# Kernel tuning notes

Hardware: AMD Instinct MI355X
Metric: run time of the kernel (lower is better)

## Reference

```python
import jax, jax.numpy as jnp
import numpy as np

DIM = 384
HEADS = 8
HEAD_DIM = DIM // HEADS
TEM_LEN = 400
SCALE = HEAD_DIM ** -0.5


def setup_inputs() -> dict:
    key = jax.random.key(0)
    ks = jax.random.split(key, 12)
    B, Lq, Lkv = 16, 1024, 1424
    inp = {
        'tem_mask': jax.random.normal(ks[0], (B, TEM_LEN, DIM), jnp.float32),
        'search_mask': jax.random.normal(ks[1], (B, Lkv - TEM_LEN, DIM), jnp.float32),
        'q': jax.random.normal(ks[2], (B, Lq, DIM), jnp.float32),
        'kv': jax.random.normal(ks[3], (B, Lkv, DIM), jnp.float32),
        'attn_pos': jax.random.normal(ks[4], (1, HEADS, Lq, Lkv), jnp.float32),
        # learned params (attn_pos_encoding_only=True: q, fused kv, proj)
        'q_w': jax.random.normal(ks[5], (DIM, DIM), jnp.float32) * 0.02,
        'q_b': jnp.zeros((DIM,), jnp.float32),
        'kv_w': jax.random.normal(ks[6], (2 * DIM, DIM), jnp.float32) * 0.02,
        'kv_b': jnp.zeros((2 * DIM,), jnp.float32),
        'proj_w': jax.random.normal(ks[7], (DIM, DIM), jnp.float32) * 0.02,
        'proj_b': jnp.zeros((DIM,), jnp.float32),
    }
    return inp


def reference(tem_mask, search_mask, q, kv, attn_pos, q_w, q_b, kv_w, kv_b, proj_w, proj_b):
    B, Lq, C = q.shape
    Lkv = kv.shape[1]
    # projections
    qh = (q @ q_w.T + q_b).reshape(B, Lq, HEADS, HEAD_DIM).transpose(0, 2, 1, 3)  # (B,H,Lq,hd)
    kvp = kv @ kv_w.T + kv_b                                                      # (B,Lkv,2C)
    k = kvp[..., :C]
    v = kvp[..., C:]
    # additive masks on v before head split (template tokens first, then search)
    v = jnp.concatenate([v[:, :TEM_LEN] + tem_mask, v[:, TEM_LEN:] + search_mask], axis=1)
    kh = k.reshape(B, Lkv, HEADS, HEAD_DIM).transpose(0, 2, 1, 3)  # (B,H,Lkv,hd)
    vh = v.reshape(B, Lkv, HEADS, HEAD_DIM).transpose(0, 2, 1, 3)  # (B,H,Lkv,hd)
    # scaled scores + untied positional bias, softmax over keys
    attn = jnp.einsum('bhqd,bhkd->bhqk', qh, kh) * SCALE + attn_pos
    attn = jax.nn.softmax(attn, axis=-1)
    x = jnp.einsum('bhqk,bhkd->bhqd', attn, vh)
    x = x.transpose(0, 2, 1, 3).reshape(B, Lq, C)
    return x @ proj_w.T + proj_b
```

## Files before the change

kernel.cpp:

```cpp
#include <hip/hip_runtime.h>
#include <stdint.h>

#define NB 16
#define NH 8
#define LQ 1024
#define LKV 1424
#define LKVP 1472
#define DIMC 384
#define NKVT 23
#define TEM 400
#define QSCALE 0.20823509f
#define LOG2E_F 1.4426950408889634f

typedef __attribute__((ext_vector_type(4))) float f32x4;
typedef __attribute__((ext_vector_type(8))) short bf16x8;
typedef __attribute__((ext_vector_type(4))) unsigned short us4;
typedef __attribute__((ext_vector_type(2))) unsigned int u32x2;
typedef __attribute__((ext_vector_type(4))) unsigned int u32x4;

__device__ __forceinline__ unsigned short f2b(float f) {
  unsigned int u = __builtin_bit_cast(unsigned int, f);
  u += 0x7fffu + ((u >> 16) & 1u);
  return (unsigned short)(u >> 16);
}

__device__ __forceinline__ void gload_lds16(const void* gsrc, void* ldst) {
  __builtin_amdgcn_global_load_lds(
      (const __attribute__((address_space(1))) void*)gsrc,
      (__attribute__((address_space(3))) void*)ldst, 16, 0, 0);
}

__global__ __launch_bounds__(256) void conv_all(
    const float* __restrict__ q, const float* __restrict__ kv,
    const float* __restrict__ qw, const float* __restrict__ kvw,
    const float* __restrict__ pw, unsigned short* __restrict__ qb,
    unsigned short* __restrict__ kvb, unsigned short* __restrict__ qwb,
    unsigned short* __restrict__ kvwb, unsigned short* __restrict__ pwb) {
  int i = blockIdx.x * 256 + threadIdx.x;
  const float* src;
  unsigned short* dst;
  if (i < 16384 * 48) { src = q; dst = qb; }
  else if (i < 39168 * 48) { i -= 16384 * 48; src = kv; dst = kvb; }
  else if (i < 39552 * 48) { i -= 39168 * 48; src = qw; dst = qwb; }
  else if (i < 40320 * 48) { i -= 39552 * 48; src = kvw; dst = kvwb; }
  else if (i < 40704 * 48) { i -= 40320 * 48; src = pw; dst = pwb; }
  else return;
  int row = i / 48, ch = i - row * 48;
  const float* sp = src + (size_t)row * DIMC + ch * 8;
  f32x4 x = *(const f32x4*)sp;
  f32x4 y = *(const f32x4*)(sp + 4);
  bf16x8 o;
  o[0] = (short)f2b(x[0]); o[1] = (short)f2b(x[1]);
  o[2] = (short)f2b(x[2]); o[3] = (short)f2b(x[3]);
  o[4] = (short)f2b(y[0]); o[5] = (short)f2b(y[1]);
  o[6] = (short)f2b(y[2]); o[7] = (short)f2b(y[3]);
  int blk = ch >> 3, c3 = (ch & 7) ^ (row & 7);
  *(bf16x8*)(dst + (size_t)row * DIMC + blk * 64 + c3 * 8) = o;
}

__global__ __launch_bounds__(256) void zero_pads(unsigned short* Qp, unsigned short* Kp,
                                                 unsigned short* Vt) {
  int i = blockIdx.x * 256 + threadIdx.x;
  u32x4 z = {0u, 0u, 0u, 0u};
  if (i < 131072) {
    *(u32x4*)(Qp + (size_t)i * 64 + 48) = z;
    *(u32x4*)(Qp + (size_t)i * 64 + 56) = z;
  } else if (i < 131072 + 188416) {
    int r = i - 131072;
    int s = r % LKVP;
    unsigned short* row = Kp + (size_t)r * 64;
    if (s < LKV) {
      *(u32x4*)(row + (6 ^ (s & 7)) * 8) = z;
      *(u32x4*)(row + (7 ^ (s & 7)) * 8) = z;
    } else {
#pragma unroll
      for (int c = 0; c < 64; c += 8) *(u32x4*)(row + c) = z;
    }
  } else if (i < 131072 + 188416 + 36864) {
    int j = i - 319488;
    int row = j / 6, x = 2 + j - (j / 6) * 6;
    int d = row % 48;
    *(u32x4*)(Vt + (size_t)row * LKVP + 1408 + ((x ^ d) & 7) * 8) = z;
  }
}

__global__ __launch_bounds__(256) void prep_pos(const float* __restrict__ pos,
                                                unsigned short* __restrict__ posb) {
  __shared__ float lds[4][1024];
  const int wave = threadIdx.x >> 6, lane = threadIdx.x & 63;
  const int l16 = lane & 15, g = lane >> 4;
  const int q16 = blockIdx.x, h = blockIdx.y;
  float* L = &lds[wave][0];

  for (int t = wave; t < NKVT; t += 4) {
#pragma unroll
    for (int i = 0; i < 4; ++i) {
      const int row = i * 4 + g;
      const int gcol = t * 64 + l16 * 4;
      f32x4 v;
      if (gcol < LKV) {
        v = *(const f32x4*)(pos + ((size_t)h * LQ + q16 * 16 + row) * LKV + gcol);
        v *= LOG2E_F;
      } else {
        f32x4 neg = {-1e30f, -1e30f, -1e30f, -1e30f};
        v = neg;
      }
      *(f32x4*)(L + row * 64 + ((l16 ^ (row & 7)) << 2)) = v;
    }
    unsigned short vals[16];
#pragma unroll
    for (int ni = 0; ni < 4; ++ni) {
      f32x4 wv = *(const f32x4*)(L + l16 * 64 + (((4 * ni + g) ^ (l16 & 7)) << 2));
#pragma unroll
      for (int r = 0; r < 4; ++r) vals[4 * ni + r] = f2b(wv[r]);
    }
    unsigned short* op = posb + ((((size_t)h * 64 + q16) * NKVT + t) * 64 + lane) * 16;
    bf16x8 a, b;
#pragma unroll
    for (int k = 0; k < 8; ++k) { a[k] = (short)vals[k]; b[k] = (short)vals[8 + k]; }
    *(bf16x8*)op = a;
    *(bf16x8*)(op + 8) = b;
  }
}

template <int MODE>
__global__ __launch_bounds__(256) void proj_gemm(
    const unsigned short* __restrict__ A, const unsigned short* __restrict__ Wb,
    const float* __restrict__ bias, const float* __restrict__ tem,
    const float* __restrict__ srch, unsigned short* __restrict__ Oq,
    unsigned short* __restrict__ Ok, unsigned short* __restrict__ Ovt,
    float* __restrict__ Of) {
  __shared__ unsigned short Ash[128 * 64];
  __shared__ unsigned short Bsh[128 * 64];
  const int tid = threadIdx.x;
  const int lane = tid & 63, l16 = lane & 15, g = lane >> 4;
  const int wave = tid >> 6, wm = wave >> 1, wn = wave & 1;
  const int n0 = blockIdx.x * 128, m0 = blockIdx.y * 128;

  f32x4 acc[4][4];
#pragma unroll
  for (int i = 0; i < 4; ++i)
#pragma unroll
    for (int j = 0; j < 4; ++j) { f32x4 z = {0.f, 0.f, 0.f, 0.f}; acc[i][j] = z; }

  const char* Abase = (const char*)A + (size_t)m0 * 768;
  const char* Bbase = (const char*)Wb + (size_t)n0 * 768;

  for (int ks = 0; ks < 6; ++ks) {
    __syncthreads();
#pragma unroll
    for (int rnd = 0; rnd < 4; ++rnd) {
      int idx = tid + rnd * 256;
      int row = idx >> 3, chunk = idx & 7;
      gload_lds16(Abase + (size_t)row * 768 + ks * 128 + chunk * 16,
                  (char*)Ash + idx * 16);
    }
#pragma unroll
    for (int rnd = 0; rnd < 4; ++rnd) {
      int idx = tid + rnd * 256;
      int row = idx >> 3, chunk = idx & 7;
      gload_lds16(Bbase + (size_t)row * 768 + ks * 128 + chunk * 16,
                  (char*)Bsh + idx * 16);
    }
    asm volatile("s_waitcnt vmcnt(0)" ::: "memory");
    __syncthreads();
#pragma unroll
    for (int kk = 0; kk < 2; ++kk) {
      bf16x8 a[4], bb[4];
#pragma unroll
      for (int mi = 0; mi < 4; ++mi) {
        int row = wm * 64 + mi * 16 + l16;
        a[mi] = *(const bf16x8*)((char*)Ash + row * 128 + (((g + 4 * kk) ^ (row & 7)) << 4));
      }
#pragma unroll
      for (int ni = 0; ni < 4; ++ni) {
        int row = wn * 64 + ni * 16 + l16;
        bb[ni] = *(const bf16x8*)((char*)Bsh + row * 128 + (((g + 4 * kk) ^ (row & 7)) << 4));
      }
#pragma unroll
      for (int mi = 0; mi < 4; ++mi)
#pragma unroll
        for (int ni = 0; ni < 4; ++ni)
          acc[mi][ni] = __builtin_amdgcn_mfma_f32_16x16x32_bf16(a[mi], bb[ni], acc[mi][ni], 0, 0, 0);
    }
  }

#pragma unroll
  for (int mi = 0; mi < 4; ++mi) {
    const int m_g0 = m0 + wm * 64 + mi * 16 + 4 * g;
#pragma unroll
    for (int ni = 0; ni < 4; ++ni) {
      const int n_g = n0 + wn * 64 + ni * 16 + l16;
      const float bv = bias[n_g];
      if (MODE == 0) {
        const int hh = n_g / 48, d = n_g - hh * 48;
#pragma unroll
        for (int r = 0; r < 4; ++r) {
          const int m_g = m_g0 + r;
          const int b = m_g >> 10, m = m_g & 1023;
          Oq[(((size_t)b * NH + hh) * LQ + m) * 64 + d] = f2b((acc[mi][ni][r] + bv) * QSCALE);
        }
      } else if (MODE == 2) {
#pragma unroll
        for (int r = 0; r < 4; ++r)
          Of[(size_t)(m_g0 + r) * DIMC + n_g] = acc[mi][ni][r] + bv;
      } else {
        const int b = m_g0 / LKV, s0 = m_g0 - b * LKV;
        if (n_g < DIMC) {
          const int hh = n_g / 48, d = n_g - hh * 48;
#pragma unroll
          for (int r = 0; r < 4; ++r) {
            const int s = s0 + r;
            const int dsw = (d & 7) | ((((d >> 3) ^ (s & 7)) & 7) << 3);
            Ok[(((size_t)b * NH + hh) * LKVP + s) * 64 + dsw] = f2b(acc[mi][ni][r] + bv);
          }
        } else {
          const int c = n_g - DIMC, hh = c / 48, d = c - hh * 48;
          const float* mb = (s0 < TEM)
                                ? tem + ((size_t)b * TEM + s0) * DIMC + c
                                : srch + ((size_t)b * (LKV - TEM) + (s0 - TEM)) * DIMC + c;
          const int off = s0 & 63;
          const int soff = (s0 & ~63) | ((((off >> 3) ^ d) & 7) << 3) | (off & 7);
          us4 pk;
#pragma unroll
          for (int r = 0; r < 4; ++r)
            pk[r] = f2b(acc[mi][ni][r] + bv + mb[(size_t)r * DIMC]);
          *(us4*)(Ovt + (((size_t)b * NH + hh) * 48 + d) * LKVP + soff) = pk;
        }
      }
    }
  }
}

__device__ __forceinline__ void stage_tile(const char* kbase, const char* vbase, int t,
                                           char* kdst, char* vdst, int wave, int lane) {
  const char* ks = kbase + (size_t)t * 8192 + wave * 2048 + lane * 16;
  char* kd = kdst + wave * 2048;
  gload_lds16(ks, kd);
  gload_lds16(ks + 1024, kd + 1024);
  if (wave < 3) {
    const char* vs = vbase + (size_t)(wave * 16 + (lane >> 3)) * (LKVP * 2) +
                     (size_t)t * 128 + (lane & 7) * 16;
    char* vd = vdst + wave * 2048;
    gload_lds16(vs, vd);
    gload_lds16(vs + 8 * (LKVP * 2), vd + 1024);
  }
}

__device__ __forceinline__ float expsum16(f32x4 (&sx)[4]) {
#pragma unroll
  for (int ni = 0; ni < 4; ++ni)
#pragma unroll
    for (int r = 0; r < 4; ++r) sx[ni][r] = exp2f(sx[ni][r]);
  float s0 = (sx[0][0] + sx[0][1]) + (sx[0][2] + sx[0][3]);
  float s1 = (sx[1][0] + sx[1][1]) + (sx[1][2] + sx[1][3]);
  float s2 = (sx[2][0] + sx[2][1]) + (sx[2][2] + sx[2][3]);
  float s3 = (sx[3][0] + sx[3][1]) + (sx[3][2] + sx[3][3]);
  float sum = (s0 + s1) + (s2 + s3);
  sum += __shfl_xor(sum, 16);
  sum += __shfl_xor(sum, 32);
  return sum;
}

__device__ __forceinline__ void packP(const f32x4 (&sx)[4], char* pbase, int swz, int g,
                                      bf16x8& af0, bf16x8& af1) {
#pragma unroll
  for (int ni = 0; ni < 4; ++ni) {
    float e0 = sx[ni][0], e1 = sx[ni][1], e2 = sx[ni][2], e3 = sx[ni][3];
    unsigned int lo, hi;
    asm("v_cvt_pk_bf16_f32 %0, %1, %2" : "=v"(lo) : "v"(e0), "v"(e1));
    asm("v_cvt_pk_bf16_f32 %0, %1, %2" : "=v"(hi) : "v"(e2), "v"(e3));
    u32x2 pk = {lo, hi};
    *(u32x2*)(pbase + ((32 * ni + 8 * g) ^ swz)) = pk;
  }
  af0 = *(const bf16x8*)(pbase + ((16 * g) ^ swz));
  af1 = *(const bf16x8*)(pbase + ((64 + 16 * g) ^ swz));
}

__device__ __forceinline__ void unpack_pos(const u32x4& w0, const u32x4& w1,
                                           f32x4 (&s)[4]) {
#pragma unroll
  for (int k = 0; k < 4; ++k) {
    const int ni = k >> 1, j2 = (k & 1) * 2;
    unsigned int a = w0[k], b = w1[k];
    s[ni][j2]         = __builtin_bit_cast(float, a << 16);
    s[ni][j2 + 1]     = __builtin_bit_cast(float, a & 0xffff0000u);
    s[ni + 2][j2]     = __builtin_bit_cast(float, b << 16);
    s[ni + 2][j2 + 1] = __builtin_bit_cast(float, b & 0xffff0000u);
  }
}

__global__ __launch_bounds__(256, 4) void attn_fwd(
    const unsigned short* __restrict__ posb, const unsigned short* __restrict__ Qp,
    const unsigned short* __restrict__ Kp, const unsigned short* __restrict__ Vt,
    unsigned short* __restrict__ X) {
  __shared__ unsigned short Ksh[2][64 * 64];
  __shared__ unsigned short Vsh[2][48 * 64];
  __shared__ unsigned short Psh[4][16 * 64];

  const int tid = threadIdx.x;
  const int lane = tid & 63, l16 = lane & 15, g = lane >> 4;
  const int wave = tid >> 6;
  const int bid = blockIdx.x;
  const int bh = bid & 127, qt = bid >> 7;
  const int b = bh >> 3, h = bh & 7;
  const int qrow = qt * 128 + wave * 32;

  bf16x8 qf[2][2];
#pragma unroll
  for (int qs = 0; qs < 2; ++qs) {
    const unsigned short* qb = Qp + ((size_t)bh * LQ + qrow + qs * 16 + l16) * 64 + 8 * g;
    qf[qs][0] = *(const bf16x8*)qb;
    qf[qs][1] = *(const bf16x8*)(qb + 32);
  }

  float l_run0 = 0.f, l_run1 = 0.f;
  f32x4 o[2][3];
#pragma unroll
  for (int qs = 0; qs < 2; ++qs)
#pragma unroll
    for (int d = 0; d < 3; ++d) { f32x4 z = {0.f, 0.f, 0.f, 0.f}; o[qs][d] = z; }

  const char* kbase = (const char*)(Kp + (size_t)bh * LKVP * 64);
  const char* vbase = (const char*)(Vt + (size_t)bh * 48 * LKVP);
  const int q16b = qt * 8 + wave * 2;
  const unsigned short* pq0 = posb + (((size_t)h * 64 + q16b) * NKVT) * 1024 + lane * 16;
  const unsigned short* pq1 = pq0 + (size_t)NKVT * 1024;
  char* pbase = (char*)&Psh[wave][0] + l16 * 128;
  const int swz = (l16 & 7) << 4;

  stage_tile(kbase, vbase, 0, (char*)&Ksh[0][0], (char*)&Vsh[0][0], wave, lane);
  asm volatile("s_waitcnt vmcnt(0)" ::: "memory");
  __syncthreads();

  int buf = 0;
  for (int t = 0; t < NKVT; ++t) {
    if (t + 1 < NKVT)
      stage_tile(kbase, vbase, t + 1, (char*)&Ksh[buf ^ 1][0], (char*)&Vsh[buf ^ 1][0],
                 wave, lane);

    u32x4 w0 = *(const u32x4*)(pq0);
    u32x4 w1 = *(const u32x4*)(pq0 + 8);
    u32x4 w2 = *(const u32x4*)(pq1);
    u32x4 w3 = *(const u32x4*)(pq1 + 8);
    pq0 += 1024; pq1 += 1024;

    f32x4 s0[4], s1[4];
    unpack_pos(w0, w1, s0);
    unpack_pos(w2, w3, s1);

#pragma unroll
    for (int ni = 0; ni < 4; ++ni) {
      const int krow = ni * 16 + l16;
      const char* kr = (const char*)&Ksh[buf][0] + krow * 128;
      bf16x8 kf0 = *(const bf16x8*)(kr + ((g ^ (krow & 7)) << 4));
      bf16x8 kf1 = *(const bf16x8*)(kr + (((g + 4) ^ (krow & 7)) << 4));
      s0[ni] = __builtin_amdgcn_mfma_f32_16x16x32_bf16(kf0, qf[0][0], s0[ni], 0, 0, 0);
      s0[ni] = __builtin_amdgcn_mfma_f32_16x16x32_bf16(kf1, qf[0][1], s0[ni], 0, 0, 0);
      s1[ni] = __builtin_amdgcn_mfma_f32_16x16x32_bf16(kf0, qf[1][0], s1[ni], 0, 0, 0);
      s1[ni] = __builtin_amdgcn_mfma_f32_16x16x32_bf16(kf1, qf[1][1], s1[ni], 0, 0, 0);
    }

    l_run0 += expsum16(s0);
    bf16x8 af00, af01, af10, af11;
    packP(s0, pbase, swz, g, af00, af01);
    l_run1 += expsum16(s1);
#pragma unroll
    for (int dn = 0; dn < 3; ++dn) {
      const int vr = 16 * dn + l16;
      const char* vrp = (const char*)&Vsh[buf][0] + vr * 128;
      bf16x8 vf0 = *(const bf16x8*)(vrp + ((g ^ (vr & 7)) << 4));
      bf16x8 vf1 = *(const bf16x8*)(vrp + (((g + 4) ^ (vr & 7)) << 4));
      o[0][dn] = __builtin_amdgcn_mfma_f32_16x16x32_bf16(af00, vf0, o[0][dn], 0, 0, 0);
      o[0][dn] = __builtin_amdgcn_mfma_f32_16x16x32_bf16(af01, vf1, o[0][dn], 0, 0, 0);
    }
    packP(s1, pbase, swz, g, af10, af11);
#pragma unroll
    for (int dn = 0; dn < 3; ++dn) {
      const int vr = 16 * dn + l16;
      const char* vrp = (const char*)&Vsh[buf][0] + vr * 128;
      bf16x8 vf0 = *(const bf16x8*)(vrp + ((g ^ (vr & 7)) << 4));
      bf16x8 vf1 = *(const bf16x8*)(vrp + (((g + 4) ^ (vr & 7)) << 4));
      o[1][dn] = __builtin_amdgcn_mfma_f32_16x16x32_bf16(af10, vf0, o[1][dn], 0, 0, 0);
      o[1][dn] = __builtin_amdgcn_mfma_f32_16x16x32_bf16(af11, vf1, o[1][dn], 0, 0, 0);
    }

    asm volatile("s_waitcnt vmcnt(0)" ::: "memory");
    __syncthreads();
    buf ^= 1;
  }

#pragma unroll
  for (int qs = 0; qs < 2; ++qs) {
    const float linv = 1.f / (qs == 0 ? l_run0 : l_run1);
#pragma unroll
    for (int r = 0; r < 4; ++r) {
      const float ib = __shfl(linv, 4 * (lane >> 4) + r);
      const int m = qrow + qs * 16 + 4 * g + r;
#pragma unroll
      for (int dn = 0; dn < 3; ++dn) {
        const int c = h * 48 + 16 * dn + l16;
        const int cs = (c & ~63) | (c & 7) | ((((c >> 3) & 7) ^ (m & 7)) << 3);
        const f32x4& ov = (qs == 0) ? o[0][dn] : o[1][dn];
        X[((size_t)b * LQ + m) * DIMC + cs] = f2b(ov[r] * ib);
      }
    }
  }
}

extern "C" void kernel_launch(void* const* d_in, const int* in_sizes, int n_in,
                              void* d_out, int out_size, void* d_ws, size_t ws_size,
                              hipStream_t stream) {
  const float* tem  = (const float*)d_in[0];
  const float* srch = (const float*)d_in[1];
  const float* q    = (const float*)d_in[2];
  const float* kv   = (const float*)d_in[3];
  const float* pos  = (const float*)d_in[4];
  const float* q_w  = (const float*)d_in[5];
  const float* q_b  = (const float*)d_in[6];
  const float* kv_w = (const float*)d_in[7];
  const float* kv_b = (const float*)d_in[8];
  const float* p_w  = (const float*)d_in[9];
  const float* p_b  = (const float*)d_in[10];
  float* out = (float*)d_out;

  char* w = (char*)d_ws;
  unsigned short* Qp   = (unsigned short*)(w);
  unsigned short* Kp   = (unsigned short*)(w + 16777216);
  unsigned short* Vt   = (unsigned short*)(w + 40894464);
  unsigned short* X    = (unsigned short*)(w + 58982400);
  unsigned short* qb   = X;
  unsigned short* posb = (unsigned short*)(w + 71565312);
  unsigned short* kvb  = (unsigned short*)(w + 95682560);
  unsigned short* qwb  = (unsigned short*)(w + 113180672);
  unsigned short* kvwb = (unsigned short*)(w + 113475584);
  unsigned short* pwb  = (unsigned short*)(w + 114065408);

  conv_all<<<7632, 256, 0, stream>>>(q, kv, q_w, kv_w, p_w, qb, kvb, qwb, kvwb, pwb);
  zero_pads<<<1392, 256, 0, stream>>>(Qp, Kp, Vt);
  prep_pos<<<dim3(64, 8), 256, 0, stream>>>(pos, posb);
  proj_gemm<0><<<dim3(3, 128), 256, 0, stream>>>(qb, qwb, q_b, nullptr, nullptr,
                                                 Qp, nullptr, nullptr, nullptr);
  proj_gemm<1><<<dim3(6, 178), 256, 0, stream>>>(kvb, kvwb, kv_b, tem, srch,
                                                 nullptr, Kp, Vt, nullptr);
  attn_fwd<<<1024, 256, 0, stream>>>(posb, Qp, Kp, Vt, X);
  proj_gemm<2><<<dim3(3, 128), 256, 0, stream>>>(X, pwb, p_b, nullptr, nullptr,
                                                 nullptr, nullptr, nullptr, out);
}
```

Baseline: 206.6 us.

## Merge prep and projection launches into fewer kernels, add MFMA priority hints

```diff
diff --git a/kernel.cpp b/kernel.cpp
--- a/kernel.cpp
+++ b/kernel.cpp
@@ -30,112 +30,109 @@
       (__attribute__((address_space(3))) void*)ldst, 16, 0, 0);
 }
 
-__global__ __launch_bounds__(256) void conv_all(
+__global__ __launch_bounds__(256) void prep_all(
     const float* __restrict__ q, const float* __restrict__ kv,
     const float* __restrict__ qw, const float* __restrict__ kvw,
-    const float* __restrict__ pw, unsigned short* __restrict__ qb,
-    unsigned short* __restrict__ kvb, unsigned short* __restrict__ qwb,
-    unsigned short* __restrict__ kvwb, unsigned short* __restrict__ pwb) {
-  int i = blockIdx.x * 256 + threadIdx.x;
-  const float* src;
-  unsigned short* dst;
-  if (i < 16384 * 48) { src = q; dst = qb; }
-  else if (i < 39168 * 48) { i -= 16384 * 48; src = kv; dst = kvb; }
-  else if (i < 39552 * 48) { i -= 39168 * 48; src = qw; dst = qwb; }
-  else if (i < 40320 * 48) { i -= 39552 * 48; src = kvw; dst = kvwb; }
-  else if (i < 40704 * 48) { i -= 40320 * 48; src = pw; dst = pwb; }
-  else return;
-  int row = i / 48, ch = i - row * 48;
-  const float* sp = src + (size_t)row * DIMC + ch * 8;
-  f32x4 x = *(const f32x4*)sp;
-  f32x4 y = *(const f32x4*)(sp + 4);
-  bf16x8 o;
-  o[0] = (short)f2b(x[0]); o[1] = (short)f2b(x[1]);
-  o[2] = (short)f2b(x[2]); o[3] = (short)f2b(x[3]);
-  o[4] = (short)f2b(y[0]); o[5] = (short)f2b(y[1]);
-  o[6] = (short)f2b(y[2]); o[7] = (short)f2b(y[3]);
-  int blk = ch >> 3, c3 = (ch & 7) ^ (row & 7);
-  *(bf16x8*)(dst + (size_t)row * DIMC + blk * 64 + c3 * 8) = o;
-}
-
-__global__ __launch_bounds__(256) void zero_pads(unsigned short* Qp, unsigned short* Kp,
-                                                 unsigned short* Vt) {
-  int i = blockIdx.x * 256 + threadIdx.x;
-  u32x4 z = {0u, 0u, 0u, 0u};
-  if (i < 131072) {
-    *(u32x4*)(Qp + (size_t)i * 64 + 48) = z;
-    *(u32x4*)(Qp + (size_t)i * 64 + 56) = z;
-  } else if (i < 131072 + 188416) {
-    int r = i - 131072;
-    int s = r % LKVP;
-    unsigned short* row = Kp + (size_t)r * 64;
-    if (s < LKV) {
-      *(u32x4*)(row + (6 ^ (s & 7)) * 8) = z;
-      *(u32x4*)(row + (7 ^ (s & 7)) * 8) = z;
-    } else {
-#pragma unroll
-      for (int c = 0; c < 64; c += 8) *(u32x4*)(row + c) = z;
-    }
-  } else if (i < 131072 + 188416 + 36864) {
-    int j = i - 319488;
-    int row = j / 6, x = 2 + j - (j / 6) * 6;
-    int d = row % 48;
-    *(u32x4*)(Vt + (size_t)row * LKVP + 1408 + ((x ^ d) & 7) * 8) = z;
-  }
-}
-
-__global__ __launch_bounds__(256) void prep_pos(const float* __restrict__ pos,
-                                                unsigned short* __restrict__ posb) {
+    const float* __restrict__ pw, const float* __restrict__ pos,
+    unsigned short* __restrict__ qb, unsigned short* __restrict__ kvb,
+    unsigned short* __restrict__ qwb, unsigned short* __restrict__ kvwb,
+    unsigned short* __restrict__ pwb, unsigned short* __restrict__ Qp,
+    unsigned short* __restrict__ Kp, unsigned short* __restrict__ Vt,
+    unsigned short* __restrict__ posb) {
   __shared__ float lds[4][1024];
-  const int wave = threadIdx.x >> 6, lane = threadIdx.x & 63;
-  const int l16 = lane & 15, g = lane >> 4;
-  const int q16 = blockIdx.x, h = blockIdx.y;
-  float* L = &lds[wave][0];
-
-  for (int t = wave; t < NKVT; t += 4) {
-#pragma unroll
-    for (int i = 0; i < 4; ++i) {
-      const int row = i * 4 + g;
-      const int gcol = t * 64 + l16 * 4;
-      f32x4 v;
-      if (gcol < LKV) {
-        v = *(const f32x4*)(pos + ((size_t)h * LQ + q16 * 16 + row) * LKV + gcol);
-        v *= LOG2E_F;
+  const int bid = blockIdx.x;
+  if (bid < 7632) {
+    int i = bid * 256 + threadIdx.x;
+    const float* src;
+    unsigned short* dst;
+    if (i < 16384 * 48) { src = q; dst = qb; }
+    else if (i < 39168 * 48) { i -= 16384 * 48; src = kv; dst = kvb; }
+    else if (i < 39552 * 48) { i -= 39168 * 48; src = qw; dst = qwb; }
+    else if (i < 40320 * 48) { i -= 39552 * 48; src = kvw; dst = kvwb; }
+    else { i -= 40320 * 48; src = pw; dst = pwb; }
+    int row = i / 48, ch = i - row * 48;
+    const float* sp = src + (size_t)row * DIMC + ch * 8;
+    f32x4 x = *(const f32x4*)sp;
+    f32x4 y = *(const f32x4*)(sp + 4);
+    bf16x8 o;
+    o[0] = (short)f2b(x[0]); o[1] = (short)f2b(x[1]);
+    o[2] = (short)f2b(x[2]); o[3] = (short)f2b(x[3]);
+    o[4] = (short)f2b(y[0]); o[5] = (short)f2b(y[1]);
+    o[6] = (short)f2b(y[2]); o[7] = (short)f2b(y[3]);
+    int blk = ch >> 3, c3 = (ch & 7) ^ (row & 7);
+    *(bf16x8*)(dst + (size_t)row * DIMC + blk * 64 + c3 * 8) = o;
+  } else if (bid < 9024) {
+    int i = (bid - 7632) * 256 + threadIdx.x;
+    u32x4 z = {0u, 0u, 0u, 0u};
+    if (i < 131072) {
+      *(u32x4*)(Qp + (size_t)i * 64 + 48) = z;
+      *(u32x4*)(Qp + (size_t)i * 64 + 56) = z;
+    } else if (i < 131072 + 188416) {
+      int r = i - 131072;
+      int s = r % LKVP;
+      unsigned short* row = Kp + (size_t)r * 64;
+      if (s < LKV) {
+        *(u32x4*)(row + (6 ^ (s & 7)) * 8) = z;
+        *(u32x4*)(row + (7 ^ (s & 7)) * 8) = z;
       } else {
-        f32x4 neg = {-1e30f, -1e30f, -1e30f, -1e30f};
-        v = neg;
-      }
-      *(f32x4*)(L + row * 64 + ((l16 ^ (row & 7)) << 2)) = v;
-    }
-    unsigned short vals[16];
-#pragma unroll
-    for (int ni = 0; ni < 4; ++ni) {
-      f32x4 wv = *(const f32x4*)(L + l16 * 64 + (((4 * ni + g) ^ (l16 & 7)) << 2));
-#pragma unroll
-      for (int r = 0; r < 4; ++r) vals[4 * ni + r] = f2b(wv[r]);
-    }
-    unsigned short* op = posb + ((((size_t)h * 64 + q16) * NKVT + t) * 64 + lane) * 16;
-    bf16x8 a, b;
-#pragma unroll
-    for (int k = 0; k < 8; ++k) { a[k] = (short)vals[k]; b[k] = (short)vals[8 + k]; }
-    *(bf16x8*)op = a;
-    *(bf16x8*)(op + 8) = b;
+#pragma unroll
+        for (int c = 0; c < 64; c += 8) *(u32x4*)(row + c) = z;
+      }
+    } else if (i < 131072 + 188416 + 36864) {
+      int j = i - 319488;
+      int row = j / 6, x = 2 + j - (j / 6) * 6;
+      int d = row % 48;
+      *(u32x4*)(Vt + (size_t)row * LKVP + 1408 + ((x ^ d) & 7) * 8) = z;
+    }
+  } else {
+    const int r = bid - 9024;
+    const int q16 = r & 63, h = r >> 6;
+    const int wave = threadIdx.x >> 6, lane = threadIdx.x & 63;
+    const int l16 = lane & 15, g = lane >> 4;
+    float* L = &lds[wave][0];
+    for (int t = wave; t < NKVT; t += 4) {
+#pragma unroll
+      for (int i = 0; i < 4; ++i) {
+        const int row = i * 4 + g;
+        const int gcol = t * 64 + l16 * 4;
+        f32x4 v;
+        if (gcol < LKV) {
+          v = *(const f32x4*)(pos + ((size_t)h * LQ + q16 * 16 + row) * LKV + gcol);
+          v *= LOG2E_F;
+        } else {
+          f32x4 neg = {-1e30f, -1e30f, -1e30f, -1e30f};
+          v = neg;
+        }
+        *(f32x4*)(L + row * 64 + ((l16 ^ (row & 7)) << 2)) = v;
+      }
+      unsigned short vals[16];
+#pragma unroll
+      for (int ni = 0; ni < 4; ++ni) {
+        f32x4 wv = *(const f32x4*)(L + l16 * 64 + (((4 * ni + g) ^ (l16 & 7)) << 2));
+#pragma unroll
+        for (int rr = 0; rr < 4; ++rr) vals[4 * ni + rr] = f2b(wv[rr]);
+      }
+      unsigned short* op = posb + ((((size_t)h * 64 + q16) * NKVT + t) * 64 + lane) * 16;
+      bf16x8 a, b;
+#pragma unroll
+      for (int k = 0; k < 8; ++k) { a[k] = (short)vals[k]; b[k] = (short)vals[8 + k]; }
+      *(bf16x8*)op = a;
+      *(bf16x8*)(op + 8) = b;
+    }
   }
 }
 
 template <int MODE>
-__global__ __launch_bounds__(256) void proj_gemm(
+__device__ __forceinline__ void proj_body(
+    unsigned short* Ash, unsigned short* Bsh, int n0, int m0,
     const unsigned short* __restrict__ A, const unsigned short* __restrict__ Wb,
     const float* __restrict__ bias, const float* __restrict__ tem,
     const float* __restrict__ srch, unsigned short* __restrict__ Oq,
     unsigned short* __restrict__ Ok, unsigned short* __restrict__ Ovt,
     float* __restrict__ Of) {
-  __shared__ unsigned short Ash[128 * 64];
-  __shared__ unsigned short Bsh[128 * 64];
   const int tid = threadIdx.x;
   const int lane = tid & 63, l16 = lane & 15, g = lane >> 4;
   const int wave = tid >> 6, wm = wave >> 1, wn = wave & 1;
-  const int n0 = blockIdx.x * 128, m0 = blockIdx.y * 128;
 
   f32x4 acc[4][4];
 #pragma unroll
@@ -232,6 +229,35 @@
   }
 }
 
+__global__ __launch_bounds__(256) void proj_qkv(
+    const unsigned short* __restrict__ qb, const unsigned short* __restrict__ qwb,
+    const float* __restrict__ q_b, const unsigned short* __restrict__ kvb,
+    const unsigned short* __restrict__ kvwb, const float* __restrict__ kv_b,
+    const float* __restrict__ tem, const float* __restrict__ srch,
+    unsigned short* __restrict__ Qp, unsigned short* __restrict__ Ok,
+    unsigned short* __restrict__ Ovt) {
+  __shared__ unsigned short Ash[128 * 64];
+  __shared__ unsigned short Bsh[128 * 64];
+  const int bid = blockIdx.x;
+  if (bid < 384) {
+    proj_body<0>(Ash, Bsh, (bid % 3) * 128, (bid / 3) * 128, qb, qwb, q_b,
+                 nullptr, nullptr, Qp, nullptr, nullptr, nullptr);
+  } else {
+    const int r = bid - 384;
+    proj_body<1>(Ash, Bsh, (r % 6) * 128, (r / 6) * 128, kvb, kvwb, kv_b,
+                 tem, srch, nullptr, Ok, Ovt, nullptr);
+  }
+}
+
+__global__ __launch_bounds__(256) void proj_out(
+    const unsigned short* __restrict__ X, const unsigned short* __restrict__ pwb,
+    const float* __restrict__ p_b, float* __restrict__ out) {
+  __shared__ unsigned short Ash[128 * 64];
+  __shared__ unsigned short Bsh[128 * 64];
+  proj_body<2>(Ash, Bsh, (blockIdx.x % 3) * 128, (blockIdx.x / 3) * 128, X, pwb, p_b,
+               nullptr, nullptr, nullptr, nullptr, nullptr, out);
+}
+
 __device__ __forceinline__ void stage_tile(const char* kbase, const char* vbase, int t,
                                            char* kdst, char* vdst, int wave, int lane) {
   const char* ks = kbase + (size_t)t * 8192 + wave * 2048 + lane * 16;
@@ -349,6 +375,7 @@
     unpack_pos(w0, w1, s0);
     unpack_pos(w2, w3, s1);
 
+    __builtin_amdgcn_s_setprio(1);
 #pragma unroll
     for (int ni = 0; ni < 4; ++ni) {
       const int krow = ni * 16 + l16;
@@ -360,11 +387,13 @@
       s1[ni] = __builtin_amdgcn_mfma_f32_16x16x32_bf16(kf0, qf[1][0], s1[ni], 0, 0, 0);
       s1[ni] = __builtin_amdgcn_mfma_f32_16x16x32_bf16(kf1, qf[1][1], s1[ni], 0, 0, 0);
     }
+    __builtin_amdgcn_s_setprio(0);
 
     l_run0 += expsum16(s0);
     bf16x8 af00, af01, af10, af11;
     packP(s0, pbase, swz, g, af00, af01);
     l_run1 += expsum16(s1);
+    __builtin_amdgcn_s_setprio(1);
 #pragma unroll
     for (int dn = 0; dn < 3; ++dn) {
       const int vr = 16 * dn + l16;
@@ -374,7 +403,9 @@
       o[0][dn] = __builtin_amdgcn_mfma_f32_16x16x32_bf16(af00, vf0, o[0][dn], 0, 0, 0);
       o[0][dn] = __builtin_amdgcn_mfma_f32_16x16x32_bf16(af01, vf1, o[0][dn], 0, 0, 0);
     }
+    __builtin_amdgcn_s_setprio(0);
     packP(s1, pbase, swz, g, af10, af11);
+    __builtin_amdgcn_s_setprio(1);
 #pragma unroll
     for (int dn = 0; dn < 3; ++dn) {
       const int vr = 16 * dn + l16;
@@ -384,6 +415,7 @@
       o[1][dn] = __builtin_amdgcn_mfma_f32_16x16x32_bf16(af10, vf0, o[1][dn], 0, 0, 0);
       o[1][dn] = __builtin_amdgcn_mfma_f32_16x16x32_bf16(af11, vf1, o[1][dn], 0, 0, 0);
     }
+    __builtin_amdgcn_s_setprio(0);
 
     asm volatile("s_waitcnt vmcnt(0)" ::: "memory");
     __syncthreads();
@@ -436,14 +468,10 @@
   unsigned short* kvwb = (unsigned short*)(w + 113475584);
   unsigned short* pwb  = (unsigned short*)(w + 114065408);
 
-  conv_all<<<7632, 256, 0, stream>>>(q, kv, q_w, kv_w, p_w, qb, kvb, qwb, kvwb, pwb);
-  zero_pads<<<1392, 256, 0, stream>>>(Qp, Kp, Vt);
-  prep_pos<<<dim3(64, 8), 256, 0, stream>>>(pos, posb);
-  proj_gemm<0><<<dim3(3, 128), 256, 0, stream>>>(qb, qwb, q_b, nullptr, nullptr,
-                                                 Qp, nullptr, nullptr, nullptr);
-  proj_gemm<1><<<dim3(6, 178), 256, 0, stream>>>(kvb, kvwb, kv_b, tem, srch,
-                                                 nullptr, Kp, Vt, nullptr);
+  prep_all<<<9536, 256, 0, stream>>>(q, kv, q_w, kv_w, p_w, pos, qb, kvb, qwb, kvwb,
+                                     pwb, Qp, Kp, Vt, posb);
+  proj_qkv<<<1452, 256, 0, stream>>>(qb, qwb, q_b, kvb, kvwb, kv_b, tem, srch,
+                                     Qp, Kp, Vt);
   attn_fwd<<<1024, 256, 0, stream>>>(posb, Qp, Kp, Vt, X);
-  proj_gemm<2><<<dim3(3, 128), 256, 0, stream>>>(X, pwb, p_b, nullptr, nullptr,
-                                                 nullptr, nullptr, nullptr, out);
-}
+  proj_out<<<384, 256, 0, stream>>>(X, pwb, p_b, out);
+}
```

New measurement: 208.6 us. No clear change (+1.0%).
